# Performance work log

Measured on AMD Instinct MI355X. Metric: run time of the kernel, lower is better.

## Reference

```python
import jax, jax.numpy as jnp
import numpy as np

N = 20000      # nodes
E = 320000     # edges (avg degree 16)
G = 200        # graphs
H = 128        # hidden_dim
LAT = 256      # latent_dim (time embedding)
L = 4          # num_layers
MAXA = 100     # max_atoms
NF = 10        # sinusoid frequencies
DIS = NF * 2 * 3
EIN = 2 * H + 9 + DIS


def setup_inputs() -> dict:
    ks = jax.random.split(jax.random.key(0), 24)
    s = 0.05
    return {
        "atom_types": jax.random.randint(ks[0], (N,), 1, MAXA),
        "t": jax.random.uniform(ks[1], (N,), dtype=jnp.float32),
        "frac_coords": jax.random.uniform(ks[2], (N, 3), dtype=jnp.float32),
        "edge_index": jax.random.randint(ks[3], (2, E), 0, N),
        "lattices": jax.random.normal(ks[4], (G, 3, 3), dtype=jnp.float32),
        "node2graph": jnp.sort(jax.random.randint(ks[5], (N,), 0, G)),
        "embed": jax.random.normal(ks[6], (MAXA, H)) * s,
        "lat_w": jax.random.normal(ks[7], (H + LAT, H)) * s,
        "lat_b": jnp.zeros((H,), jnp.float32),
        "edge_w1": jax.random.normal(ks[8], (L, EIN, H)) * s,
        "edge_b1": jnp.zeros((L, H), jnp.float32),
        "edge_w2": jax.random.normal(ks[9], (L, H, H)) * s,
        "edge_b2": jnp.zeros((L, H), jnp.float32),
        "node_w1": jax.random.normal(ks[10], (L, 2 * H, H)) * s,
        "node_b1": jnp.zeros((L, H), jnp.float32),
        "node_w2": jax.random.normal(ks[11], (L, H, H)) * s,
        "node_b2": jnp.zeros((L, H), jnp.float32),
        "coord_w1": jax.random.normal(ks[12], (H, H)) * s,
        "coord_b1": jnp.zeros((H,), jnp.float32),
        "coord_w2": jax.random.normal(ks[13], (H, 1)) * s,
    }


def _seg_mean(x, idx, n):
    # scatter-mean with dim_size=n (torch_scatter semantics: empty segments -> 0)
    s = jax.ops.segment_sum(x, idx, num_segments=n)
    c = jax.ops.segment_sum(jnp.ones((idx.shape[0], 1), x.dtype), idx, num_segments=n)
    return s / jnp.maximum(c, 1.0)


def reference(atom_types, t, frac_coords, edge_index, lattices, node2graph,
              embed, lat_w, lat_b, edge_w1, edge_b1, edge_w2, edge_b2,
              node_w1, node_b1, node_w2, node_b2, coord_w1, coord_b1, coord_w2):
    silu = jax.nn.silu
    ei0, ei1 = edge_index[0], edge_index[1]
    shift = frac_coords[ei1] - frac_coords[ei0]
    frac_diff = shift - jnp.floor(shift + 0.5 + 1e-4)             # [E,3] min-image convention
    e2g = node2graph[ei0]                                          # [E]
    # sinusoidal time embedding -> [N, LAT]
    half = LAT // 2
    fr = jnp.exp(jnp.arange(half, dtype=jnp.float32) * (-np.log(10000.0) / (half - 1)))
    te = t[:, None] * fr[None, :]
    t_emb = jnp.concatenate([jnp.sin(te), jnp.cos(te)], axis=-1)
    # atom embedding + latent projection -> [N, H]
    h = jnp.concatenate([embed[atom_types - 1], t_emb], axis=-1) @ lat_w + lat_b
    # sinusoid distance embedding -> [E, DIS]
    freqs = 2.0 * np.pi * jnp.arange(NF, dtype=jnp.float32)
    de = (frac_diff[..., None] * freqs).reshape(-1, 3 * NF)
    dis = jnp.concatenate([jnp.sin(de), jnp.cos(de)], axis=-1)
    # lattice inner products, gathered per edge -> [E, 9]
    lat_ip = jnp.einsum('gij,gkj->gik', lattices, lattices).reshape(-1, 9)[e2g]
    ef = None
    for i in range(L):
        hij = jnp.concatenate([h[ei0], h[ei1], lat_ip, dis], axis=-1)   # [E, EIN]
        ef = silu(silu(hij @ edge_w1[i] + edge_b1[i]) @ edge_w2[i] + edge_b2[i])
        agg = _seg_mean(ef, ei1, N)
        h = h + silu(silu(jnp.concatenate([h, agg], axis=-1) @ node_w1[i] + node_b1[i]) @ node_w2[i] + node_b2[i])
    gate = silu(ef @ coord_w1 + coord_b1) @ coord_w2                    # [E,1]
    return _seg_mean(frac_diff * gate, ei1, N)                          # [N,3]
```

## Files before the change

kernel.cpp:

```cpp
#include <hip/hip_runtime.h>
#include <hip/hip_bf16.h>
#include <hip/hip_fp16.h>
#include <math.h>

#define HD    128
#define EIN   325
#define PST   136
#define DST   72
#define NST   264
#define XST   136
#define IST   408

typedef _Float16 half8 __attribute__((ext_vector_type(8)));
typedef _Float16 half4 __attribute__((ext_vector_type(4)));
typedef _Float16 half2v __attribute__((ext_vector_type(2)));
typedef float    floatx16 __attribute__((ext_vector_type(16)));

#define WSYNC() __asm__ volatile("s_waitcnt lgkmcnt(0)" ::: "memory")

__device__ __forceinline__ float silu_f(float x) {
    return x * __builtin_amdgcn_rcpf(1.0f + __expf(-x));
}

__device__ __forceinline__ void wfrag_elem(
    const float* __restrict__ src, _Float16* __restrict__ dst,
    int r_all, int Ktot, int krow0, int Kact, int nks, int mode)
{
    int per = nks * 2048;
    int m = r_all / per, r = r_all - m * per;
    int j    = r & 7;
    int lane = (r >> 3) & 63;
    int blk  = r >> 9;
    int ks = blk >> 2, sub = blk & 3;
    int l31 = lane & 31, lh = lane >> 5;
    int k   = 16 * ks + 8 * lh + j;
    int col;
    if (mode == 0)      col = 4 * l31 + sub;
    else if (mode == 1) col = (sub >> 1) * 64 + 2 * l31 + (sub & 1);
    else                col = sub * 32 + l31;
    float v = (k < Kact) ? src[(size_t)m * Ktot * HD + (size_t)(krow0 + k) * HD + col] : 0.f;
    dst[r_all] = (_Float16)v;
}

__global__ void k_wprep_all(
    const float* __restrict__ ew1, const float* __restrict__ ew2,
    const float* __restrict__ nw1, const float* __restrict__ nw2,
    const float* __restrict__ cw1, const float* __restrict__ lat_w,
    _Float16* __restrict__ w1aT, _Float16* __restrict__ w1bT,
    _Float16* __restrict__ wdT,  _Float16* __restrict__ w2T,
    _Float16* __restrict__ nw1T, _Float16* __restrict__ nw2T,
    _Float16* __restrict__ cw1T, _Float16* __restrict__ latwT)
{
    int b = blockIdx.x;
    int t = threadIdx.x;
    if (b < 256)       { wfrag_elem(ew1,  w1aT, (b       ) * 256 + t, EIN, 0,   128, 8,  0); }
    else if (b < 512)  { wfrag_elem(ew1,  w1bT, (b -  256) * 256 + t, EIN, 128, 128, 8,  0); }
    else if (b < 640)  { wfrag_elem(ew1,  wdT,  (b -  512) * 256 + t, EIN, 265, 60,  4,  0); }
    else if (b < 896)  { wfrag_elem(ew2,  w2T,  (b -  640) * 256 + t, HD,  0,   128, 8,  0); }
    else if (b < 1280) { wfrag_elem(nw1,  nw1T, (b -  896) * 256 + t, 256, 0,   256, 16, 2); }
    else if (b < 1472) { wfrag_elem(nw2,  nw2T, (b - 1280) * 256 + t, HD,  0,   128, 8,  2); }
    else if (b < 1536) { wfrag_elem(cw1,  cw1T, (b - 1472) * 256 + t, HD,  0,   128, 8,  0); }
    else               { wfrag_elem(lat_w, latwT,(b - 1536) * 256 + t, 384, 0,  384, 25, 1); }
}

__global__ void k_hist(const int* __restrict__ ei1, int* __restrict__ cnt, int E) {
    int idx = blockIdx.x * 256 + threadIdx.x;
    if (idx < E) atomicAdd(&cnt[ei1[idx]], 1);
}

__global__ __launch_bounds__(1024) void k_scan(const int* __restrict__ cnt,
                                               int* __restrict__ head,
                                               float* __restrict__ deginv, int N) {
    __shared__ int part[1024];
    int tid = threadIdx.x;
    int chunk = (N + 1023) >> 10;
    int start = tid * chunk, stop = min(start + chunk, N);
    int s = 0;
    for (int i = start; i < stop; ++i) s += cnt[i];
    part[tid] = s;
    __syncthreads();
    for (int off = 1; off < 1024; off <<= 1) {
        int v = (tid >= off) ? part[tid - off] : 0;
        __syncthreads();
        part[tid] += v;
        __syncthreads();
    }
    int run = (tid > 0) ? part[tid - 1] : 0;
    for (int i = start; i < stop; ++i) {
        head[i] = run;
        int c = cnt[i];
        run += c;
        deginv[i] = 1.0f / fmaxf((float)c, 1.0f);
    }
}

__global__ void k_scatter(const int* __restrict__ ei1, int* __restrict__ head,
                          int* __restrict__ perm, int E) {
    int e = blockIdx.x * 256 + threadIdx.x;
    if (e < E) {
        int d = ei1[e];
        int pos = atomicAdd(&head[d], 1);
        perm[pos] = e;
    }
}

__global__ void k_esort(const int* __restrict__ ei, const int* __restrict__ n2g,
                        const float* __restrict__ fc, const int* __restrict__ perm,
                        int* __restrict__ eaS, int* __restrict__ ebS, int* __restrict__ egS,
                        float* __restrict__ fdS, int E) {
    int s = blockIdx.x * 256 + threadIdx.x;
    if (s >= E) return;
    int e = perm[s];
    int a = ei[e], b = ei[E + e];
    eaS[s] = a; ebS[s] = b; egS[s] = n2g[a];
    #pragma unroll
    for (int d = 0; d < 3; ++d) {
        float sh = fc[b * 3 + d] - fc[a * 3 + d];
        fdS[s * 3 + d] = sh - floorf(sh + 0.5f + 1e-4f);
    }
}

__global__ void k_rlat(const float* __restrict__ lat, const float* __restrict__ ew1,
                       const float* __restrict__ eb1, _Float16* __restrict__ R16, int G) {
    int idx = blockIdx.x * 256 + threadIdx.x;
    if (idx >= 4 * G * HD) return;
    int l = idx / (G * HD), r = idx - l * (G * HD), g = r >> 7, c = r & 127;
    const float* L = lat + g * 9;
    const float* W = ew1 + (size_t)l * EIN * HD + 256 * HD;
    float s = eb1[l * HD + c];
    #pragma unroll
    for (int i = 0; i < 3; ++i)
        #pragma unroll
        for (int k = 0; k < 3; ++k) {
            float lp = L[i*3+0]*L[k*3+0] + L[i*3+1]*L[k*3+1] + L[i*3+2]*L[k*3+2];
            s = fmaf(lp, W[(i * 3 + k) * HD + c], s);
        }
    R16[idx] = (_Float16)s;
}

__global__ void k_fin(const float* __restrict__ outsum, const float* __restrict__ deginv,
                      float* __restrict__ out, int N) {
    int idx = blockIdx.x * 256 + threadIdx.x;
    if (idx < N * 3) out[idx] = outsum[idx] * deginv[idx / 3];
}

__global__ __launch_bounds__(256) void k_init_pq(
    const int* __restrict__ at, const float* __restrict__ t,
    const float* __restrict__ embed, const _Float16* __restrict__ latwF,
    const float* __restrict__ lat_b, float* __restrict__ h,
    _Float16* __restrict__ h16,
    const _Float16* __restrict__ WaF, const _Float16* __restrict__ WbF,
    _Float16* __restrict__ P16, _Float16* __restrict__ Q16, int N)
{
    __shared__ __align__(16) _Float16 xs[64 * IST];
    __shared__ int   atL[64];
    __shared__ float tL[64];
    __shared__ float frL[128];
    int tid = threadIdx.x;
    int n0  = blockIdx.x * 64;

    if (tid < 64) {
        int node = n0 + tid;
        atL[tid] = (node < N) ? at[node] - 1 : 0;
        tL[tid]  = (node < N) ? t[node] : 0.f;
    }
    if (tid < 128) frL[tid] = __expf(-(float)tid * 0.07252236514f);
    __syncthreads();

    for (int c = tid; c < 64 * 32; c += 256) {
        int row = c >> 5, p = c & 31;
        float4 v = {0, 0, 0, 0};
        if (n0 + row < N) v = *(const float4*)(embed + (size_t)atL[row] * HD + p * 4);
        _Float16* d = xs + row * IST + p * 4;
        d[0] = (_Float16)v.x; d[1] = (_Float16)v.y; d[2] = (_Float16)v.z; d[3] = (_Float16)v.w;
    }
    for (int c = tid; c < 64 * 272; c += 256) {
        int row = c / 272, j = c - row * 272;
        float v = 0.f;
        if (j < 256 && n0 + row < N) {
            int k = j & 127;
            float a = tL[row] * frL[k];
            v = (j < 128) ? __sinf(a) : __cosf(a);
        }
        xs[row * IST + 128 + j] = (_Float16)v;
    }
    __syncthreads();

    int lane = tid & 63, wv = tid >> 6;
    int l31 = lane & 31, lh = lane >> 5;
    int rm = (wv >> 1) * 32, cb = (wv & 1) * 64;
    int n0c = cb + 2 * l31, n1c = n0c + 1;

    floatx16 acc0 = {}, acc1 = {};
    {
        const _Float16* ap = xs + (size_t)(rm + l31) * IST + lh * 8;
        const _Float16* bp = latwF + (size_t)(wv & 1) * 1024 + lane * 8;
        for (int ks = 0; ks < 25; ++ks) {
            half8 a  = *(const half8*)(ap + ks * 16);
            acc0 = __builtin_amdgcn_mfma_f32_32x32x16_f16(a, *(const half8*)(bp + ks * 2048), acc0, 0, 0, 0);
            acc1 = __builtin_amdgcn_mfma_f32_32x32x16_f16(a, *(const half8*)(bp + ks * 2048 + 512), acc1, 0, 0, 0);
        }
    }
    __syncthreads();

    {
        float2 bb = *(const float2*)(lat_b + n0c);
        #pragma unroll
        for (int r = 0; r < 16; ++r) {
            int row = rm + (r & 3) + 8 * (r >> 2) + 4 * lh;
            int node = n0 + row;
            float v0 = acc0[r] + bb.x, v1 = acc1[r] + bb.y;
            half2v h2; h2[0] = (_Float16)v0; h2[1] = (_Float16)v1;
            if (node < N) {
                *(float2*)(h + (size_t)node * HD + n0c) = make_float2(v0, v1);
                *(half2v*)(h16 + (size_t)node * HD + n0c) = h2;
            }
            *(half2v*)(xs + row * PST + n0c) = h2;
        }
    }
    __syncthreads();

    {
        const _Float16* BT  = (wv & 1) ? WbF : WaF;
        _Float16*       OUT = (wv & 1) ? Q16 : P16;
        floatx16 acc[4] = {};
        const _Float16* ap = xs + (size_t)(rm + l31) * PST + lh * 8;
        const _Float16* bp = BT + (size_t)lane * 8;
        for (int ks = 0; ks < 8; ++ks) {
            half8 a = *(const half8*)(ap + ks * 16);
            #pragma unroll
            for (int i = 0; i < 4; ++i) {
                half8 b = *(const half8*)(bp + ks * 2048 + i * 512);
                acc[i] = __builtin_amdgcn_mfma_f32_32x32x16_f16(a, b, acc[i], 0, 0, 0);
            }
        }
        #pragma unroll
        for (int r = 0; r < 16; ++r) {
            int row = rm + (r & 3) + 8 * (r >> 2) + 4 * lh;
            int node = n0 + row;
            if (node < N) {
                half4 o;
                #pragma unroll
                for (int i = 0; i < 4; ++i) o[i] = (_Float16)acc[i][r];
                *(half4*)(OUT + (size_t)node * HD + 4 * l31) = o;
            }
        }
    }
}

template <bool LAST>
__global__ __launch_bounds__(256, 4) void k_edge(
    const int* __restrict__ eaS, const int* __restrict__ ebS,
    const int* __restrict__ egS, const float* __restrict__ fdS,
    const _Float16* __restrict__ P16, const _Float16* __restrict__ Q16,
    const _Float16* __restrict__ R16, const _Float16* __restrict__ WdT,
    const _Float16* __restrict__ W2T, const float* __restrict__ b2,
    const _Float16* __restrict__ cw1T, const float* __restrict__ cb1,
    const float* __restrict__ cw2,
    float* __restrict__ aggsum, float* __restrict__ outsum, int E)
{
    __shared__ __align__(16) _Float16 xt[4][32 * PST];
    __shared__ int   eaW[4][32], ebW[4][32], egW[4][32];
    __shared__ float fdW[LAST ? 4 : 1][32][3];
    __shared__ float gateW[LAST ? 4 : 1][32];

    int tid  = threadIdx.x;
    int wv   = tid >> 6, lane = tid & 63;
    int l31  = lane & 31, lh = lane >> 5;
    int s0   = blockIdx.x * 128 + wv * 32;

    _Float16* XT  = xt[wv];
    int* eaw = eaW[wv];
    int* ebw = ebW[wv];
    int* egw = egW[wv];

    const _Float16* bwd = WdT  + (size_t)lane * 8;
    const _Float16* bw2 = W2T  + (size_t)lane * 8;

    if (lane < 32) {
        int s = s0 + lane;
        int a = 0, b = -1, g = 0;
        if (s < E) { a = eaS[s]; b = ebS[s]; g = egS[s]; }
        eaw[lane] = a; ebw[lane] = b; egw[lane] = g;
        if (LAST) {
            float f0 = 0.f, f1 = 0.f, f2 = 0.f;
            if (s < E) { f0 = fdS[s*3]; f1 = fdS[s*3+1]; f2 = fdS[s*3+2]; }
            fdW[wv][lane][0] = f0; fdW[wv][lane][1] = f1; fdW[wv][lane][2] = f2;
        }
    }

    {
        int s = s0 + l31;
        float fd3[3] = {0.f, 0.f, 0.f};
        if (s < E) { fd3[0] = fdS[s*3]; fd3[1] = fdS[s*3+1]; fd3[2] = fdS[s*3+2]; }
        _Float16* dr = XT + l31 * DST + lh * 30;
        #pragma unroll
        for (int d = 0; d < 3; ++d) {
            float ang = 6.283185307179586f * fd3[d];
            float s1 = __sinf(ang), c1 = __cosf(ang);
            float tc = 2.f * c1;
            float m2 = lh ? 1.f : 0.f;
            float m1 = lh ? c1  : s1;
            half2v h01; h01[0] = (_Float16)m2; h01[1] = (_Float16)m1;
            *(half2v*)(dr + 10 * d) = h01;
            #pragma unroll
            for (int w = 2; w < 10; w += 2) {
                float a0 = tc * m1 - m2;
                float a1 = tc * a0 - m1;
                half2v hh; hh[0] = (_Float16)a0; hh[1] = (_Float16)a1;
                *(half2v*)(dr + 10 * d + w) = hh;
                m2 = a0; m1 = a1;
            }
        }
        half2v z; z[0] = (_Float16)0.f; z[1] = (_Float16)0.f;
        *(half2v*)(XT + l31 * DST + 60) = z;
        *(half2v*)(XT + l31 * DST + 62) = z;
    }
    WSYNC();

    half8 af[4];
    {
        const _Float16* dp = XT + l31 * DST + lh * 8;
        af[0] = *(const half8*)(dp);      af[1] = *(const half8*)(dp + 16);
        af[2] = *(const half8*)(dp + 32); af[3] = *(const half8*)(dp + 48);
    }
    WSYNC();

    #pragma unroll 4
    for (int k = 0; k < 8; ++k) {
        int c   = lane + 64 * k;
        int row = c >> 4, p8 = (c & 15) * 8;
        int a = eaw[row];
        int b = ebw[row]; if (b < 0) b = 0;
        int g = egw[row];
        half8 pv = *(const half8*)(P16 + (size_t)a * HD + p8);
        half8 qv = *(const half8*)(Q16 + (size_t)b * HD + p8);
        half8 rv = *(const half8*)(R16 + (size_t)g * HD + p8);
        *(half8*)(XT + row * PST + p8) = pv + qv + rv;
    }

    floatx16 acc[4] = {};
    #pragma unroll
    for (int ks = 0; ks < 4; ++ks) {
        #pragma unroll
        for (int i = 0; i < 4; ++i) {
            half8 b = *(const half8*)(bwd + (((ks << 2) | i) << 9));
            acc[i] = __builtin_amdgcn_mfma_f32_32x32x16_f16(af[ks], b, acc[i], 0, 0, 0);
        }
    }
    WSYNC();

    #pragma unroll
    for (int r = 0; r < 16; ++r) {
        int row = (r & 3) + 8 * (r >> 2) + 4 * lh;
        half4 pq = *(const half4*)(XT + row * PST + 4 * l31);
        half4 o;
        #pragma unroll
        for (int i = 0; i < 4; ++i)
            o[i] = (_Float16)silu_f(acc[i][r] + (float)pq[i]);
        *(half4*)(XT + row * PST + 4 * l31) = o;
    }
    WSYNC();

    #pragma unroll
    for (int i = 0; i < 4; ++i) acc[i] = (floatx16){};
    for (int ks = 0; ks < 8; ++ks) {
        half8 a = *(const half8*)(XT + (size_t)l31 * PST + ks * 16 + lh * 8);
        #pragma unroll
        for (int i = 0; i < 4; ++i) {
            half8 b = *(const half8*)(bw2 + (((ks << 2) | i) << 9));
            acc[i] = __builtin_amdgcn_mfma_f32_32x32x16_f16(a, b, acc[i], 0, 0, 0);
        }
    }
    {
        float4 b2v = *(const float4*)(b2 + 4 * l31);
        #pragma unroll
        for (int r = 0; r < 16; ++r) {
            int row = (r & 3) + 8 * (r >> 2) + 4 * lh;
            half4 o;
            o[0] = (_Float16)silu_f(acc[0][r] + b2v.x);
            o[1] = (_Float16)silu_f(acc[1][r] + b2v.y);
            o[2] = (_Float16)silu_f(acc[2][r] + b2v.z);
            o[3] = (_Float16)silu_f(acc[3][r] + b2v.w);
            *(half4*)(XT + row * PST + 4 * l31) = o;
        }
    }
    WSYNC();

    if (!LAST) {
        int c2 = lane * 2;
        float sx = 0.f, sy = 0.f;
        int cur = -1;
        for (int r = 0; r < 32; ++r) {
            int d = ebw[r];
            half2v v = *(const half2v*)(XT + r * PST + c2);
            float vx = (float)v[0], vy = (float)v[1];
            if (d != cur) {
                if (cur >= 0) {
                    atomicAdd(&aggsum[(size_t)cur * HD + c2],     sx);
                    atomicAdd(&aggsum[(size_t)cur * HD + c2 + 1], sy);
                }
                cur = d; sx = vx; sy = vy;
            } else { sx += vx; sy += vy; }
        }
        if (cur >= 0) {
            atomicAdd(&aggsum[(size_t)cur * HD + c2],     sx);
            atomicAdd(&aggsum[(size_t)cur * HD + c2 + 1], sy);
        }
    } else {
        const _Float16* bw3 = cw1T + (size_t)lane * 8;
        #pragma unroll
        for (int i = 0; i < 4; ++i) acc[i] = (floatx16){};
        for (int ks = 0; ks < 8; ++ks) {
            half8 a = *(const half8*)(XT + (size_t)l31 * PST + ks * 16 + lh * 8);
            #pragma unroll
            for (int i = 0; i < 4; ++i) {
                half8 b = *(const half8*)(bw3 + (((ks << 2) | i) << 9));
                acc[i] = __builtin_amdgcn_mfma_f32_32x32x16_f16(a, b, acc[i], 0, 0, 0);
            }
        }
        float4 cbv = *(const float4*)(cb1 + 4 * l31);
        float4 wv4 = *(const float4*)(cw2 + 4 * l31);
        #pragma unroll
        for (int r = 0; r < 16; ++r) {
            float p = silu_f(acc[0][r] + cbv.x) * wv4.x
                    + silu_f(acc[1][r] + cbv.y) * wv4.y
                    + silu_f(acc[2][r] + cbv.z) * wv4.z
                    + silu_f(acc[3][r] + cbv.w) * wv4.w;
            p += __shfl_xor(p, 16);
            p += __shfl_xor(p, 8);
            p += __shfl_xor(p, 4);
            p += __shfl_xor(p, 2);
            p += __shfl_xor(p, 1);
            if (l31 == 0) {
                int row = (r & 3) + 8 * (r >> 2) + 4 * lh;
                gateW[wv][row] = p;
            }
        }
        WSYNC();
        if (lane < 32) {
            int r = lane, d = ebw[r];
            if (d >= 0 && (r == 0 || ebw[r - 1] != d)) {
                float sx = 0.f, sy = 0.f, sz = 0.f;
                for (int q = r; q < 32 && ebw[q] == d; ++q) {
                    float g = gateW[wv][q];
                    sx += fdW[wv][q][0] * g;
                    sy += fdW[wv][q][1] * g;
                    sz += fdW[wv][q][2] * g;
                }
                atomicAdd(&outsum[d * 3 + 0], sx);
                atomicAdd(&outsum[d * 3 + 1], sy);
                atomicAdd(&outsum[d * 3 + 2], sz);
            }
        }
    }
}

__global__ __launch_bounds__(256) void k_node_pq(
    float* __restrict__ h, _Float16* __restrict__ h16,
    float* __restrict__ aggsum, const float* __restrict__ deginv,
    const _Float16* __restrict__ W1F, const float* __restrict__ b1,
    const _Float16* __restrict__ W2F, const float* __restrict__ b2,
    const _Float16* __restrict__ WaF, const _Float16* __restrict__ WbF,
    _Float16* __restrict__ P16, _Float16* __restrict__ Q16, int N)
{
    __shared__ __align__(16) _Float16 xs[32 * NST];
    _Float16* x1s = xs;

    int tid = threadIdx.x;
    int n0  = blockIdx.x * 32;

    for (int c = tid; c < 32 * 16; c += 256) {
        int row = c >> 4, p = c & 15;
        int node = n0 + row;
        uint4 v = {0, 0, 0, 0};
        if (node < N) v = *(const uint4*)(h16 + (size_t)node * HD + p * 8);
        *(uint4*)(xs + row * NST + p * 8) = v;
    }
    for (int c = tid; c < 32 * 32; c += 256) {
        int row = c >> 5, q = c & 31;
        int node = n0 + row;
        float4 v = {0, 0, 0, 0};
        float di = 0.f;
        if (node < N) {
            size_t gi = (size_t)node * HD + q * 4;
            v = *(float4*)(aggsum + gi);
            *(float4*)(aggsum + gi) = make_float4(0.f, 0.f, 0.f, 0.f);
            di = deginv[node];
        }
        half4 o;
        o[0] = (_Float16)(v.x * di); o[1] = (_Float16)(v.y * di);
        o[2] = (_Float16)(v.z * di); o[3] = (_Float16)(v.w * di);
        *(half4*)(xs + row * NST + HD + q * 4) = o;
    }
    __syncthreads();

    int lane = tid & 63, wv = tid >> 6;
    int l31 = lane & 31, lh = lane >> 5;
    int nc  = wv * 32 + l31;

    floatx16 acc0 = {};
    {
        const _Float16* ap = xs + (size_t)l31 * NST + lh * 8;
        const _Float16* bp = W1F + (size_t)wv * 512 + lane * 8;
        for (int ks = 0; ks < 16; ++ks) {
            half8 a = *(const half8*)(ap + ks * 16);
            acc0 = __builtin_amdgcn_mfma_f32_32x32x16_f16(a, *(const half8*)(bp + ks * 2048), acc0, 0, 0, 0);
        }
    }
    __syncthreads();
    {
        float b10 = b1[nc];
        #pragma unroll
        for (int r = 0; r < 16; ++r) {
            int row = (r & 3) + 8 * (r >> 2) + 4 * lh;
            x1s[row * XST + nc] = (_Float16)silu_f(acc0[r] + b10);
        }
    }
    __syncthreads();

    acc0 = {};
    {
        const _Float16* ap = x1s + (size_t)l31 * XST + lh * 8;
        const _Float16* bp = W2F + (size_t)wv * 512 + lane * 8;
        for (int ks = 0; ks < 8; ++ks) {
            half8 a = *(const half8*)(ap + ks * 16);
            acc0 = __builtin_amdgcn_mfma_f32_32x32x16_f16(a, *(const half8*)(bp + ks * 2048), acc0, 0, 0, 0);
        }
    }
    __syncthreads();

    {
        float b20 = b2[nc];
        #pragma unroll
        for (int r = 0; r < 16; ++r) {
            int row = (r & 3) + 8 * (r >> 2) + 4 * lh;
            int node = n0 + row;
            float v0 = silu_f(acc0[r] + b20);
            _Float16 hv;
            if (node < N) {
                size_t g0 = (size_t)node * HD + nc;
                v0 += h[g0];
                h[g0] = v0;
                hv = (_Float16)v0;
                h16[g0] = hv;
            } else hv = (_Float16)0.f;
            xs[row * PST + nc] = hv;
        }
    }
    __syncthreads();

    {
        const _Float16* BT  = (wv >> 1) ? WbF : WaF;
        _Float16*       OUT = (wv >> 1) ? Q16 : P16;
        int sp = 2 * (wv & 1);
        int c0 = 4 * l31 + sp;
        floatx16 a0 = {}, a1 = {};
        const _Float16* bp = BT + (size_t)sp * 512 + lane * 8;
        const _Float16* ap = xs + (size_t)l31 * PST + lh * 8;
        for (int ks = 0; ks < 8; ++ks) {
            half8 a = *(const half8*)(ap + ks * 16);
            a0 = __builtin_amdgcn_mfma_f32_32x32x16_f16(a, *(const half8*)(bp + ks * 2048), a0, 0, 0, 0);
            a1 = __builtin_amdgcn_mfma_f32_32x32x16_f16(a, *(const half8*)(bp + ks * 2048 + 512), a1, 0, 0, 0);
        }
        #pragma unroll
        for (int r = 0; r < 16; ++r) {
            int row = (r & 3) + 8 * (r >> 2) + 4 * lh;
            int node = n0 + row;
            if (node < N) {
                half2v o; o[0] = (_Float16)a0[r]; o[1] = (_Float16)a1[r];
                *(half2v*)(OUT + (size_t)node * HD + c0) = o;
            }
        }
    }
}

extern "C" void kernel_launch(void* const* d_in, const int* in_sizes, int n_in,
                              void* d_out, int out_size, void* d_ws, size_t ws_size,
                              hipStream_t stream)
{
    const int*   at    = (const int*)  d_in[0];
    const float* t     = (const float*)d_in[1];
    const float* fc    = (const float*)d_in[2];
    const int*   ei    = (const int*)  d_in[3];
    const float* lat   = (const float*)d_in[4];
    const int*   n2g   = (const int*)  d_in[5];
    const float* embed = (const float*)d_in[6];
    const float* lat_w = (const float*)d_in[7];
    const float* lat_b = (const float*)d_in[8];
    const float* ew1   = (const float*)d_in[9];
    const float* eb1   = (const float*)d_in[10];
    const float* ew2   = (const float*)d_in[11];
    const float* eb2   = (const float*)d_in[12];
    const float* nw1   = (const float*)d_in[13];
    const float* nb1   = (const float*)d_in[14];
    const float* nw2   = (const float*)d_in[15];
    const float* nb2   = (const float*)d_in[16];
    const float* cw1   = (const float*)d_in[17];
    const float* cb1   = (const float*)d_in[18];
    const float* cw2   = (const float*)d_in[19];

    int N = in_sizes[0];
    int E = in_sizes[3] / 2;
    int G = in_sizes[4] / 9;

    char* p = (char*)d_ws;
    float* h      = (float*)p;  p += (size_t)N * HD * 4;
    float* aggsum = (float*)p;  p += (size_t)N * HD * 4;
    float* outsum = (float*)p;  p += (size_t)N * 3 * 4;
    int*   cnt    = (int*)p;    p += (size_t)N * 4;
    int*   head   = (int*)p;    p += (size_t)N * 4;
    float* deginv = (float*)p;  p += (size_t)N * 4;
    int*   perm   = (int*)p;    p += (size_t)E * 4;
    int*   eaS    = (int*)p;    p += (size_t)E * 4;
    int*   ebS    = (int*)p;    p += (size_t)E * 4;
    int*   egS    = (int*)p;    p += (size_t)E * 4;
    float* fdS    = (float*)p;  p += (size_t)E * 3 * 4;
    _Float16* h16   = (_Float16*)p; p += (size_t)N * HD * 2;
    _Float16* P16   = (_Float16*)p; p += (size_t)N * HD * 2;
    _Float16* Q16   = (_Float16*)p; p += (size_t)N * HD * 2;
    _Float16* w1aT  = (_Float16*)p; p += (size_t)4 * HD * HD * 2;
    _Float16* w1bT  = (_Float16*)p; p += (size_t)4 * HD * HD * 2;
    _Float16* wdT   = (_Float16*)p; p += (size_t)4 * HD * 64 * 2;
    _Float16* w2T   = (_Float16*)p; p += (size_t)4 * HD * HD * 2;
    _Float16* nw1T  = (_Float16*)p; p += (size_t)3 * HD * 256 * 2;
    _Float16* nw2T  = (_Float16*)p; p += (size_t)3 * HD * HD * 2;
    _Float16* cw1T  = (_Float16*)p; p += (size_t)HD * HD * 2;
    _Float16* latwT = (_Float16*)p; p += (size_t)HD * 400 * 2;
    _Float16* R16   = (_Float16*)p; p += (size_t)4 * G * HD * 2;

    hipMemsetAsync(aggsum, 0, ((size_t)N * HD + (size_t)N * 3 + N) * 4, stream);

    k_wprep_all<<<1736, 256, 0, stream>>>(ew1, ew2, nw1, nw2, cw1, lat_w,
                                          w1aT, w1bT, wdT, w2T, nw1T, nw2T, cw1T, latwT);

    k_hist   <<<(E + 255) / 256, 256, 0, stream>>>(ei + E, cnt, E);
    k_scan   <<<1, 1024, 0, stream>>>(cnt, head, deginv, N);
    k_scatter<<<(E + 255) / 256, 256, 0, stream>>>(ei + E, head, perm, E);
    k_esort  <<<(E + 255) / 256, 256, 0, stream>>>(ei, n2g, fc, perm, eaS, ebS, egS, fdS, E);
    k_rlat   <<<(4 * G * HD + 255) / 256, 256, 0, stream>>>(lat, ew1, eb1, R16, G);
    k_init_pq<<<(N + 63) / 64, 256, 0, stream>>>(at, t, embed, latwT, lat_b, h, h16,
                                                 w1aT, w1bT, P16, Q16, N);

    int eblocks = (E + 127) / 128;
    int nblocks = (N + 31) / 32;
    for (int l = 0; l < 3; ++l) {
        k_edge<false><<<eblocks, 256, 0, stream>>>(eaS, ebS, egS, fdS, P16, Q16,
            R16 + (size_t)l * G * HD, wdT + (size_t)l * HD * 64,
            w2T + (size_t)l * HD * HD, eb2 + l * HD,
            cw1T, cb1, cw2, aggsum, outsum, E);
        k_node_pq<<<nblocks, 256, 0, stream>>>(h, h16, aggsum, deginv,
            nw1T + (size_t)l * HD * 256, nb1 + l * HD,
            nw2T + (size_t)l * HD * HD,  nb2 + l * HD,
            w1aT + (size_t)(l + 1) * HD * HD, w1bT + (size_t)(l + 1) * HD * HD,
            P16, Q16, N);
    }
    k_edge<true><<<eblocks, 256, 0, stream>>>(eaS, ebS, egS, fdS, P16, Q16,
        R16 + (size_t)3 * G * HD, wdT + (size_t)3 * HD * 64,
        w2T + (size_t)3 * HD * HD, eb2 + 3 * HD,
        cw1T, cb1, cw2, aggsum, outsum, E);

    k_fin<<<(N * 3 + 255) / 256, 256, 0, stream>>>(outsum, deginv, (float*)d_out, N);
}
```

Baseline: 491.2 us.

## Gather P/Q/R rows into registers in MFMA layout, split segmented scatter by half-wave

The per-edge P+Q+R gather now loads half4 pieces straight into registers matching the MFMA accumulator layout. This removes the LDS round trip and two LDS waits before the first silu epilogue. The segmented atomic reduction now has each half-wave handle 16 rows with 4 columns per lane instead of all 32 rows with 2 columns, which shortens the serial loop but can issue more atomics when a destination run crosses the halfway point. Launch bounds drop from 4 to 3 blocks per SM to make room for the 16 half4 registers held per lane.

```diff
diff --git a/kernel.cpp b/kernel.cpp
--- a/kernel.cpp
+++ b/kernel.cpp
@@ -249,7 +249,7 @@
 }
 
 template <bool LAST>
-__global__ __launch_bounds__(256, 4) void k_edge(
+__global__ __launch_bounds__(256, 3) void k_edge(
     const int* __restrict__ eaS, const int* __restrict__ ebS,
     const int* __restrict__ egS, const float* __restrict__ fdS,
     const _Float16* __restrict__ P16, const _Float16* __restrict__ Q16,
@@ -268,6 +268,7 @@
     int wv   = tid >> 6, lane = tid & 63;
     int l31  = lane & 31, lh = lane >> 5;
     int s0   = blockIdx.x * 128 + wv * 32;
+    int q0   = 4 * l31;
 
     _Float16* XT  = xt[wv];
     int* eaw = eaW[wv];
@@ -324,19 +325,17 @@
         af[0] = *(const half8*)(dp);      af[1] = *(const half8*)(dp + 16);
         af[2] = *(const half8*)(dp + 32); af[3] = *(const half8*)(dp + 48);
     }
-    WSYNC();
-
-    #pragma unroll 4
-    for (int k = 0; k < 8; ++k) {
-        int c   = lane + 64 * k;
-        int row = c >> 4, p8 = (c & 15) * 8;
+
+    half4 pqr[16];
+    #pragma unroll
+    for (int r = 0; r < 16; ++r) {
+        int row = (r & 3) + 8 * (r >> 2) + 4 * lh;
         int a = eaw[row];
         int b = ebw[row]; if (b < 0) b = 0;
         int g = egw[row];
-        half8 pv = *(const half8*)(P16 + (size_t)a * HD + p8);
-        half8 qv = *(const half8*)(Q16 + (size_t)b * HD + p8);
-        half8 rv = *(const half8*)(R16 + (size_t)g * HD + p8);
-        *(half8*)(XT + row * PST + p8) = pv + qv + rv;
+        pqr[r] = *(const half4*)(P16 + (size_t)a * HD + q0)
+               + *(const half4*)(Q16 + (size_t)b * HD + q0)
+               + *(const half4*)(R16 + (size_t)g * HD + q0);
     }
 
     floatx16 acc[4] = {};
@@ -348,17 +347,15 @@
             acc[i] = __builtin_amdgcn_mfma_f32_32x32x16_f16(af[ks], b, acc[i], 0, 0, 0);
         }
     }
-    WSYNC();
 
     #pragma unroll
     for (int r = 0; r < 16; ++r) {
         int row = (r & 3) + 8 * (r >> 2) + 4 * lh;
-        half4 pq = *(const half4*)(XT + row * PST + 4 * l31);
         half4 o;
         #pragma unroll
         for (int i = 0; i < 4; ++i)
-            o[i] = (_Float16)silu_f(acc[i][r] + (float)pq[i]);
-        *(half4*)(XT + row * PST + 4 * l31) = o;
+            o[i] = (_Float16)silu_f(acc[i][r] + (float)pqr[r][i]);
+        *(half4*)(XT + row * PST + q0) = o;
     }
     WSYNC();
 
@@ -373,7 +370,7 @@
         }
     }
     {
-        float4 b2v = *(const float4*)(b2 + 4 * l31);
+        float4 b2v = *(const float4*)(b2 + q0);
         #pragma unroll
         for (int r = 0; r < 16; ++r) {
             int row = (r & 3) + 8 * (r >> 2) + 4 * lh;
@@ -382,30 +379,35 @@
             o[1] = (_Float16)silu_f(acc[1][r] + b2v.y);
             o[2] = (_Float16)silu_f(acc[2][r] + b2v.z);
             o[3] = (_Float16)silu_f(acc[3][r] + b2v.w);
-            *(half4*)(XT + row * PST + 4 * l31) = o;
+            *(half4*)(XT + row * PST + q0) = o;
         }
     }
     WSYNC();
 
     if (!LAST) {
-        int c2 = lane * 2;
-        float sx = 0.f, sy = 0.f;
+        int c4 = l31 * 4;
+        int r0 = lh * 16;
+        float t0 = 0.f, t1 = 0.f, t2 = 0.f, t3 = 0.f;
         int cur = -1;
-        for (int r = 0; r < 32; ++r) {
+        for (int r = r0; r < r0 + 16; ++r) {
             int d = ebw[r];
-            half2v v = *(const half2v*)(XT + r * PST + c2);
-            float vx = (float)v[0], vy = (float)v[1];
+            half4 v = *(const half4*)(XT + r * PST + c4);
             if (d != cur) {
                 if (cur >= 0) {
-                    atomicAdd(&aggsum[(size_t)cur * HD + c2],     sx);
-                    atomicAdd(&aggsum[(size_t)cur * HD + c2 + 1], sy);
+                    float* dst = aggsum + (size_t)cur * HD + c4;
+                    atomicAdd(dst + 0, t0); atomicAdd(dst + 1, t1);
+                    atomicAdd(dst + 2, t2); atomicAdd(dst + 3, t3);
                 }
-                cur = d; sx = vx; sy = vy;
-            } else { sx += vx; sy += vy; }
+                cur = d;
+                t0 = (float)v[0]; t1 = (float)v[1]; t2 = (float)v[2]; t3 = (float)v[3];
+            } else {
+                t0 += (float)v[0]; t1 += (float)v[1]; t2 += (float)v[2]; t3 += (float)v[3];
+            }
         }
         if (cur >= 0) {
-            atomicAdd(&aggsum[(size_t)cur * HD + c2],     sx);
-            atomicAdd(&aggsum[(size_t)cur * HD + c2 + 1], sy);
+            float* dst = aggsum + (size_t)cur * HD + c4;
+            atomicAdd(dst + 0, t0); atomicAdd(dst + 1, t1);
+            atomicAdd(dst + 2, t2); atomicAdd(dst + 3, t3);
         }
     } else {
         const _Float16* bw3 = cw1T + (size_t)lane * 8;
@@ -419,8 +421,8 @@
                 acc[i] = __builtin_amdgcn_mfma_f32_32x32x16_f16(a, b, acc[i], 0, 0, 0);
             }
         }
-        float4 cbv = *(const float4*)(cb1 + 4 * l31);
-        float4 wv4 = *(const float4*)(cw2 + 4 * l31);
+        float4 cbv = *(const float4*)(cb1 + q0);
+        float4 wv4 = *(const float4*)(cw2 + q0);
         #pragma unroll
         for (int r = 0; r < 16; ++r) {
             float p = silu_f(acc[0][r] + cbv.x) * wv4.x
```

After: 623.5 us. +26.9%, slower.
